# Kernel optimization log

Measured on AMD Instinct MI355X. Metric: run time of the kernel, lower is better.

## Reference

```python
import jax, jax.numpy as jnp
import numpy as np

T, B, I, H, O = 512, 128, 512, 512, 12

def setup_inputs() -> dict:
    key = jax.random.key(0)
    ks = jax.random.split(key, 17)
    def w(k, shape):
        # xavier-normal-ish init
        std = float(np.sqrt(2.0 / (shape[0] + shape[-1])))
        return jax.random.normal(k, shape, dtype=jnp.float32) * std
    return {
        "x": jax.random.normal(ks[0], (T, B, I), dtype=jnp.float32),
        "w0": w(ks[1], (O, H)), "wz": w(ks[2], (O, H)), "wr": w(ks[3], (O, H)),
        "ws": w(ks[4], (I, H)),
        "wa": w(ks[5], (H, H)), "ua": w(ks[6], (I, H)), "va": w(ks[7], (H, 1)),
        "u0": w(ks[8], (H, H)), "uz": w(ks[9], (H, H)), "ur": w(ks[10], (H, H)),
        "c0": w(ks[11], (I, H)), "cz": w(ks[12], (I, H)), "cr": w(ks[13], (I, H)),
        "fc_w": w(ks[14], (H, O)),
        "fc_b": jnp.zeros((O,), dtype=jnp.float32),
        "max_labels": 16,
    }

def reference(x, w0, wz, wr, ws, wa, ua, va, u0, uz, ur, c0, cz, cr, fc_w, fc_b, max_labels):
    # x: [T, B, I] encoder states; decode max_labels steps of a Bahdanau-attention GRU.
    s0 = jnp.tanh(x[0] @ ws)              # [B, H]
    out0 = s0 @ fc_w + fc_b               # [B, O]
    U = jnp.einsum('tbi,ih->tbh', x, ua)  # precomputed encoder projection
    va_v = va[:, 0]                       # [H]

    def step(carry, _):
        s, out = carry                                          # [B,H], [B,O]
        e = jnp.einsum('tbh,h->tb', jnp.tanh(s @ wa + U), va_v)  # [T,B] additive scores
        a = jax.nn.softmax(e, axis=0)                           # attention over T
        c = jnp.einsum('tb,tbi->bi', a, x)                      # [B,I] context
        r = jax.nn.sigmoid(out @ wr + s @ ur + c @ cr)
        z = jax.nn.sigmoid(out @ wz + s @ uz + c @ cz)
        sh = jnp.tanh(out @ w0 + (r * s) @ u0 + c @ c0)
        s_new = (1.0 - z) * s + z * sh
        out_new = s_new @ fc_w + fc_b
        return (s_new, out_new), out_new

    _, outs = jax.lax.scan(step, (s0, out0), None, length=max_labels - 1)
    all_outs = jnp.concatenate([out0[None], outs], axis=0)  # [L, B, O]
    return jnp.transpose(all_outs, (1, 0, 2))               # [B, L, O]
```

## Files before the change

### kernel.cpp

```cpp
#include <hip/hip_runtime.h>

#define NSTEP 16

typedef __attribute__((ext_vector_type(8))) short s16x8;
typedef __attribute__((ext_vector_type(4))) float f32x4;
typedef __attribute__((ext_vector_type(2))) float f32x2;

__device__ __forceinline__ float bf2f(unsigned short u){
  union { unsigned int i; float f; } v; v.i = ((unsigned int)u) << 16; return v.f;
}
__device__ __forceinline__ unsigned short f2bf(float f){
  union { float f; unsigned int i; } v; v.f = f;
  unsigned int r = v.i + 0x7fffu + ((v.i >> 16) & 1u);
  return (unsigned short)(r >> 16);
}
__device__ __forceinline__ unsigned char f2fp8(float f){
  return (unsigned char)(__builtin_amdgcn_cvt_pk_fp8_f32(f, f, 0, false) & 0xff);
}
__device__ __forceinline__ float fast_rcp(float x){ return __builtin_amdgcn_rcpf(x); }
__device__ __forceinline__ float fast_tanh(float x){
  float e = __expf(2.0f * x);
  return 1.0f - 2.0f * fast_rcp(e + 1.0f);
}
__device__ __forceinline__ float fast_sigmoid(float x){
  return fast_rcp(1.0f + __expf(-x));
}
__device__ __forceinline__ void gload16(const void* g, void* l){
  __builtin_amdgcn_global_load_lds((const __attribute__((address_space(1))) void*)g,
                                   (__attribute__((address_space(3))) void*)l, 16, 0, 0);
}
__device__ __forceinline__ float wave_sum(float v){
#pragma unroll
  for (int off = 32; off; off >>= 1) v += __shfl_xor(v, off, 64);
  return v;
}
__device__ __forceinline__ void fp8x8_dec(uint2 w, float* u){
  f32x2 d0 = __builtin_amdgcn_cvt_pk_f32_fp8(w.x, false);
  f32x2 d1 = __builtin_amdgcn_cvt_pk_f32_fp8(w.x, true);
  f32x2 d2 = __builtin_amdgcn_cvt_pk_f32_fp8(w.y, false);
  f32x2 d3 = __builtin_amdgcn_cvt_pk_f32_fp8(w.y, true);
  u[0] = d0[0]; u[1] = d0[1]; u[2] = d1[0]; u[3] = d1[1];
  u[4] = d2[0]; u[5] = d2[1]; u[6] = d3[0]; u[7] = d3[1];
}

struct GemmLDS { unsigned short A[64 * 64]; unsigned short B[128 * 64]; };

__global__ __launch_bounds__(512) void ugemm_k(
    const unsigned short* __restrict__ A, const unsigned short* __restrict__ Bt,
    unsigned char* __restrict__ o8){
  __shared__ GemmLDS lds;
  const int tid = threadIdx.x;
  const int lane = tid & 63, wid = tid >> 6;
  const int wr = wid >> 2, wc = wid & 3;
  const int mt = blockIdx.y, nt = blockIdx.x;
  f32x4 acc[2][2];
#pragma unroll
  for (int m = 0; m < 2; ++m)
#pragma unroll
    for (int n = 0; n < 2; ++n) acc[m][n] = (f32x4)0.0f;

  for (int kt = 0; kt < 512; kt += 64){
    __syncthreads();
    {
      int row = tid >> 3, kc = (tid & 7) ^ (row & 7);
      gload16(A + (size_t)(mt * 64 + row) * 512 + kt + kc * 8, &lds.A[tid * 8]);
#pragma unroll
      for (int p = 0; p < 2; ++p){
        int s = p * 512 + tid;
        int br = s >> 3, bkc = (s & 7) ^ (br & 7);
        gload16(Bt + (size_t)(nt * 128 + br) * 512 + kt + bkc * 8, &lds.B[s * 8]);
      }
    }
    __syncthreads();
#pragma unroll
    for (int ks = 0; ks < 2; ++ks){
      int kc_l = (lane >> 4) + ks * 4;
      s16x8 av[2], bv[2];
#pragma unroll
      for (int m = 0; m < 2; ++m){
        int r = wr * 32 + m * 16 + (lane & 15);
        av[m] = *(const s16x8*)&lds.A[r * 64 + ((kc_l ^ (r & 7)) << 3)];
      }
#pragma unroll
      for (int n = 0; n < 2; ++n){
        int c = wc * 32 + n * 16 + (lane & 15);
        bv[n] = *(const s16x8*)&lds.B[c * 64 + ((kc_l ^ (c & 7)) << 3)];
      }
#pragma unroll
      for (int m = 0; m < 2; ++m)
#pragma unroll
        for (int n = 0; n < 2; ++n)
          acc[m][n] = __builtin_amdgcn_mfma_f32_16x16x32_bf16(av[m], bv[n], acc[m][n], 0, 0, 0);
    }
  }
#pragma unroll
  for (int m = 0; m < 2; ++m)
#pragma unroll
    for (int n = 0; n < 2; ++n){
      int r_base = mt * 64 + wr * 32 + m * 16 + ((lane >> 4) << 2);
      int col = nt * 128 + wc * 32 + n * 16 + (lane & 15);
#pragma unroll
      for (int q = 0; q < 4; ++q)
        o8[(size_t)(r_base + q) * 512 + col] = f2fp8(acc[m][n][q]);
    }
}

struct FLDS { unsigned short A[64 * 256]; unsigned short B[64 * 256]; };

template<int EPI>
__device__ __forceinline__ void fgemm_body(int mt, int nt,
    const unsigned short* __restrict__ A, const unsigned short* __restrict__ Bt,
    unsigned short* __restrict__ ob0, float* __restrict__ o0,
    const float* __restrict__ e0, const float* __restrict__ e1,
    const float* __restrict__ e2, FLDS& lds){
  const int tid = threadIdx.x;
  const int lane = tid & 63, wid = tid >> 6;
  const int wr = wid >> 1, wc = wid & 1;
  f32x4 acc[2];
  acc[0] = (f32x4)0.0f; acc[1] = (f32x4)0.0f;

  for (int kt = 0; kt < 512; kt += 256){
    if (kt) __syncthreads();
#pragma unroll
    for (int i = 0; i < 4; ++i){
      int s = i * 512 + tid;
      int row = s >> 5, c = s & 31;
      int sc = (c & 24) | ((c & 7) ^ (row & 7));
      gload16(A + (size_t)(mt * 64 + row) * 512 + kt + sc * 8, &lds.A[s * 8]);
      gload16(Bt + (size_t)(nt * 64 + row) * 512 + kt + sc * 8, &lds.B[s * 8]);
    }
    __syncthreads();
#pragma unroll
    for (int kk = 0; kk < 8; ++kk){
      int kch = kk * 4 + (lane >> 4);
      int ar = wr * 16 + (lane & 15);
      int asw = (kch & 24) | ((kch & 7) ^ (ar & 7));
      s16x8 av = *(const s16x8*)&lds.A[ar * 256 + asw * 8];
#pragma unroll
      for (int n = 0; n < 2; ++n){
        int br = wc * 32 + n * 16 + (lane & 15);
        int bsw = (kch & 24) | ((kch & 7) ^ (br & 7));
        s16x8 bv = *(const s16x8*)&lds.B[br * 256 + bsw * 8];
        acc[n] = __builtin_amdgcn_mfma_f32_16x16x32_bf16(av, bv, acc[n], 0, 0, 0);
      }
    }
  }

#pragma unroll
  for (int n = 0; n < 2; ++n){
    int r_base = mt * 64 + wr * 16 + ((lane >> 4) << 2);
    int col = nt * 64 + wc * 32 + n * 16 + (lane & 15);
#pragma unroll
    for (int q = 0; q < 4; ++q){
      float v = acc[n][q];
      size_t r_ = (size_t)(r_base + q);
      if constexpr (EPI == 1){
        float t = fast_tanh(v);
        o0[r_ * 512 + col] = t;
        ob0[r_ * 512 + col] = f2bf(t);
      } else if constexpr (EPI == 2){
        o0[r_ * 2048 + col] = v + e0[col];
      } else if constexpr (EPI == 4){
        float v2 = v + e0[r_ * 512 + col];
        float sh = fast_tanh(v2);
        float z  = e1[r_ * 512 + col];
        float so = e2[r_ * 512 + col];
        float sn = (1.0f - z) * so + z * sh;
        o0[r_ * 512 + col] = sn;
        ob0[r_ * 512 + col] = f2bf(sn);
      }
    }
  }
}

template<int EPI>
__global__ __launch_bounds__(512) void fgemm_k(
    const unsigned short* __restrict__ A, const unsigned short* __restrict__ Bt,
    unsigned short* __restrict__ ob0, float* __restrict__ o0,
    const float* __restrict__ e0, const float* __restrict__ e1,
    const float* __restrict__ e2){
  __shared__ FLDS lds;
  fgemm_body<EPI>(blockIdx.y, blockIdx.x, A, Bt, ob0, o0, e0, e1, e2, lds);
}

__global__ __launch_bounds__(512) void ec_k(const unsigned char* __restrict__ U8,
    const unsigned char* __restrict__ x8, const float* __restrict__ pre1,
    const float* __restrict__ va, float* __restrict__ cpart, float* __restrict__ psum){
  __shared__ float cred[8][512];
  __shared__ float pred[8];
  int chunk = blockIdx.x, b = blockIdx.y;
  int tid = threadIdx.x, lane = tid & 63, wid = tid >> 6;
  const float* pp = pre1 + (size_t)b * 2048 + lane * 8;
  float4 p0 = *(const float4*)pp, p1 = *(const float4*)(pp + 4);
  const float* vp = va + lane * 8;
  float4 v0 = *(const float4*)vp, v1 = *(const float4*)(vp + 4);
  float sv[8] = {p0.x, p0.y, p0.z, p0.w, p1.x, p1.y, p1.z, p1.w};
  float vv[8] = {v0.x, v0.y, v0.z, v0.w, v1.x, v1.y, v1.z, v1.w};
  float acc[8] = {0, 0, 0, 0, 0, 0, 0, 0};
  float psum_l = 0.f;
  int t0 = chunk * 256 + wid * 32;
  for (int i = 0; i < 32; ++i){
    int t = t0 + i;
    uint2 w = *(const uint2*)(U8 + ((size_t)t * 128 + b) * 512 + lane * 8);
    float u[8];
    fp8x8_dec(w, u);
    float e = 0.f;
#pragma unroll
    for (int k = 0; k < 8; ++k)
      e += fast_tanh(u[k] + sv[k]) * vv[k];
    e = wave_sum(e);
    float p = __expf(e);
    psum_l += p;
    uint2 wx = *(const uint2*)(x8 + ((size_t)t * 128 + b) * 512 + lane * 8);
    float ux[8];
    fp8x8_dec(wx, ux);
#pragma unroll
    for (int k = 0; k < 8; ++k) acc[k] += p * ux[k];
  }
#pragma unroll
  for (int k = 0; k < 8; ++k) cred[wid][lane * 8 + k] = acc[k];
  if (lane == 0) pred[wid] = psum_l;
  __syncthreads();
  float cs = 0.f;
#pragma unroll
  for (int w = 0; w < 8; ++w) cs += cred[w][tid];
  cpart[((size_t)chunk * 128 + b) * 512 + tid] = cs;
  if (tid == 0){
    float s = 0.f;
#pragma unroll
    for (int w = 0; w < 8; ++w) s += pred[w];
    psum[chunk * 128 + b] = s;
  }
}

__global__ __launch_bounds__(512) void gates_k(
    const float* __restrict__ cpart, const float* __restrict__ psum,
    const unsigned short* __restrict__ P2w, const float* __restrict__ pre1,
    const float* __restrict__ s_prev,
    unsigned short* __restrict__ rsb, float* __restrict__ zbuf, float* __restrict__ cu0){
  __shared__ FLDS lds;
  __shared__ float rden_s[64];
  const int tid = threadIdx.x;
  const int lane = tid & 63, wid = tid >> 6;
  const int wr = wid >> 1, wc = wid & 1;
  const int nt = blockIdx.x, mt = blockIdx.y;
  if (tid < 64){
    float d = psum[mt * 64 + tid] + psum[128 + mt * 64 + tid];
    rden_s[tid] = fast_rcp(d);
  }
  f32x4 acc[2];
  acc[0] = (f32x4)0.0f; acc[1] = (f32x4)0.0f;

  for (int kt = 0; kt < 512; kt += 256){
    __syncthreads();
#pragma unroll
    for (int i = 0; i < 4; ++i){
      int s = i * 512 + tid;
      int row = s >> 5, c = s & 31;
      int sc = (c & 24) | ((c & 7) ^ (row & 7));
      int b = mt * 64 + row;
      const float* cp0 = cpart + (size_t)b * 512 + kt + sc * 8;
      const float* cp1 = cp0 + (size_t)128 * 512;
      float rd = rden_s[row];
      float4 a0 = *(const float4*)cp0, a1 = *(const float4*)(cp0 + 4);
      float4 b0 = *(const float4*)cp1, b1 = *(const float4*)(cp1 + 4);
      s16x8 t8;
      t8[0] = (short)f2bf((a0.x + b0.x) * rd); t8[1] = (short)f2bf((a0.y + b0.y) * rd);
      t8[2] = (short)f2bf((a0.z + b0.z) * rd); t8[3] = (short)f2bf((a0.w + b0.w) * rd);
      t8[4] = (short)f2bf((a1.x + b1.x) * rd); t8[5] = (short)f2bf((a1.y + b1.y) * rd);
      t8[6] = (short)f2bf((a1.z + b1.z) * rd); t8[7] = (short)f2bf((a1.w + b1.w) * rd);
      *(s16x8*)&lds.A[s * 8] = t8;
      gload16(P2w + (size_t)(nt * 64 + row) * 512 + kt + sc * 8, &lds.B[s * 8]);
    }
    __syncthreads();
#pragma unroll
    for (int kk = 0; kk < 8; ++kk){
      int kch = kk * 4 + (lane >> 4);
      int ar = wr * 16 + (lane & 15);
      int asw = (kch & 24) | ((kch & 7) ^ (ar & 7));
      s16x8 av = *(const s16x8*)&lds.A[ar * 256 + asw * 8];
#pragma unroll
      for (int n = 0; n < 2; ++n){
        int br = wc * 32 + n * 16 + (lane & 15);
        int bsw = (kch & 24) | ((kch & 7) ^ (br & 7));
        s16x8 bv = *(const s16x8*)&lds.B[br * 256 + bsw * 8];
        acc[n] = __builtin_amdgcn_mfma_f32_16x16x32_bf16(av, bv, acc[n], 0, 0, 0);
      }
    }
  }

#pragma unroll
  for (int n = 0; n < 2; ++n){
    int r_base = mt * 64 + wr * 16 + ((lane >> 4) << 2);
    int col = nt * 64 + wc * 32 + n * 16 + (lane & 15);
#pragma unroll
    for (int q = 0; q < 4; ++q){
      float v = acc[n][q];
      size_t r_ = (size_t)(r_base + q);
      float v2 = v + pre1[r_ * 2048 + 512 + col];
      if (col < 512){
        float rg = fast_sigmoid(v2);
        rsb[r_ * 512 + col] = f2bf(rg * s_prev[r_ * 512 + col]);
      } else if (col < 1024){
        zbuf[r_ * 512 + (col - 512)] = fast_sigmoid(v2);
      } else {
        cu0[r_ * 512 + (col - 1024)] = v2;
      }
    }
  }
}

__global__ __launch_bounds__(512) void dout_k(const float* __restrict__ s_hist,
    const float* __restrict__ fcwT, const float* __restrict__ fcb,
    float* __restrict__ dout){
  int lane = threadIdx.x & 63, wid = threadIdx.x >> 6;
  int w = blockIdx.x * 8 + wid;
  int step = w >> 7, b = w & 127;
  const float* sp = s_hist + (size_t)w * 512 + lane * 8;
  float4 sa = *(const float4*)sp, sb = *(const float4*)(sp + 4);
#pragma unroll
  for (int o = 0; o < 12; ++o){
    const float* fp = fcwT + (size_t)o * 512 + lane * 8;
    float4 fa = *(const float4*)fp, fb = *(const float4*)(fp + 4);
    float sum = sa.x * fa.x + sa.y * fa.y + sa.z * fa.z + sa.w * fa.w +
                sb.x * fb.x + sb.y * fb.y + sb.z * fb.z + sb.w * fb.w;
    sum = wave_sum(sum);
    if (lane == 0)
      dout[(size_t)b * (NSTEP * 12) + step * 12 + o] = sum + fcb[o];
  }
}

__global__ __launch_bounds__(256) void castx_k(const float* __restrict__ x,
    unsigned short* __restrict__ xb, unsigned char* __restrict__ x8){
  size_t idx = (size_t)blockIdx.x * 256 + threadIdx.x;
  const float* p = x + idx * 8;
  float4 a = *(const float4*)p, b = *(const float4*)(p + 4);
  s16x8 t8;
  t8[0] = (short)f2bf(a.x); t8[1] = (short)f2bf(a.y);
  t8[2] = (short)f2bf(a.z); t8[3] = (short)f2bf(a.w);
  t8[4] = (short)f2bf(b.x); t8[5] = (short)f2bf(b.y);
  t8[6] = (short)f2bf(b.z); t8[7] = (short)f2bf(b.w);
  *(s16x8*)(xb + idx * 8) = t8;
  unsigned int lo, hi;
  lo = __builtin_amdgcn_cvt_pk_fp8_f32(a.x, a.y, 0, false);
  lo = __builtin_amdgcn_cvt_pk_fp8_f32(a.z, a.w, lo, true);
  hi = __builtin_amdgcn_cvt_pk_fp8_f32(b.x, b.y, 0, false);
  hi = __builtin_amdgcn_cvt_pk_fp8_f32(b.z, b.w, hi, true);
  uint2 w; w.x = lo; w.y = hi;
  *(uint2*)(x8 + idx * 8) = w;
}

__global__ __launch_bounds__(512) void trans_k(
    const float* __restrict__ ua, const float* __restrict__ wsm,
    const float* __restrict__ u0, const float* __restrict__ wa,
    const float* __restrict__ urm, const float* __restrict__ uz,
    const float* __restrict__ cr, const float* __restrict__ cz,
    const float* __restrict__ c0, const float* __restrict__ wrm,
    const float* __restrict__ wzm, const float* __restrict__ w0m,
    const float* __restrict__ fcw, const float* __restrict__ fcb,
    unsigned short* __restrict__ Pua, unsigned short* __restrict__ Pws,
    unsigned short* __restrict__ P3w, unsigned short* __restrict__ P1w,
    unsigned short* __restrict__ P2w, float* __restrict__ fcwT,
    float* __restrict__ bias_full){
  __shared__ unsigned short tr[64][72];
  int bid = blockIdx.x, tid = threadIdx.x;
  if (bid < 640){
    int mi = bid >> 6, tile = bid & 63;
    int trr = tile >> 3, tcc = tile & 7;
    const float* src = nullptr; const float* W = nullptr; unsigned short* dst;
    switch (mi){
      case 0: src = ua;  dst = Pua;               break;
      case 1: src = wsm; dst = Pws;               break;
      case 2: src = u0;  dst = P3w;               break;
      case 3: src = wa;  dst = P1w;               break;
      case 4: src = urm; dst = P1w + 512 * 512;  W = wrm; break;
      case 5: src = uz;  dst = P1w + 1024 * 512; W = wzm; break;
      case 6: src = nullptr; dst = P1w + 1536 * 512; W = w0m; break;
      case 7: src = cr;  dst = P2w;               break;
      case 8: src = cz;  dst = P2w + 512 * 512;   break;
      default:src = c0;  dst = P2w + 1024 * 512;  break;
    }
    int r = tid >> 3, c8 = (tid & 7) * 8;
    int h = trr * 64 + r;
    float vals[8];
    if (src){
      const float* sp = src + (size_t)h * 512 + tcc * 64 + c8;
      float4 a = *(const float4*)sp, b = *(const float4*)(sp + 4);
      vals[0] = a.x; vals[1] = a.y; vals[2] = a.z; vals[3] = a.w;
      vals[4] = b.x; vals[5] = b.y; vals[6] = b.z; vals[7] = b.w;
    } else {
#pragma unroll
      for (int k = 0; k < 8; ++k) vals[k] = 0.f;
    }
    if (W){
      float fr[12];
#pragma unroll
      for (int o = 0; o < 12; ++o) fr[o] = fcw[h * 12 + o];
#pragma unroll
      for (int jj = 0; jj < 8; ++jj){
        int j = tcc * 64 + c8 + jj;
        float cj = 0.f;
#pragma unroll
        for (int o = 0; o < 12; ++o) cj += fr[o] * W[o * 512 + j];
        vals[jj] += cj;
      }
    }
    unsigned short* lp = &tr[r][c8];
#pragma unroll
    for (int k = 0; k < 8; ++k) lp[k] = f2bf(vals[k]);
    __syncthreads();
    s16x8 o8v;
#pragma unroll
    for (int k = 0; k < 8; ++k) o8v[k] = (short)tr[c8 + k][r];
    *(s16x8*)(dst + (size_t)(tcc * 64 + r) * 512 + trr * 64 + c8) = o8v;
  } else if (bid < 652){
    int gidx = (bid - 640) * 512 + tid;
    int h = gidx / 12, o = gidx - h * 12;
    fcwT[(size_t)o * 512 + h] = fcw[h * 12 + o];
  } else {
#pragma unroll
    for (int p = 0; p < 4; ++p){
      int col = p * 512 + tid;
      float v = 0.f;
      if (p > 0){
        const float* W = (p == 1) ? wrm : (p == 2) ? wzm : w0m;
#pragma unroll
        for (int o = 0; o < 12; ++o) v += fcb[o] * W[o * 512 + tid];
      }
      bias_full[col] = v;
    }
  }
}

extern "C" void kernel_launch(void* const* d_in, const int* in_sizes, int n_in,
                              void* d_out, int out_size, void* d_ws, size_t ws_size,
                              hipStream_t stream){
  const float* x   = (const float*)d_in[0];
  const float* w0  = (const float*)d_in[1];
  const float* wz  = (const float*)d_in[2];
  const float* wrm = (const float*)d_in[3];
  const float* wsm = (const float*)d_in[4];
  const float* wa  = (const float*)d_in[5];
  const float* ua  = (const float*)d_in[6];
  const float* va  = (const float*)d_in[7];
  const float* u0  = (const float*)d_in[8];
  const float* uz  = (const float*)d_in[9];
  const float* urm = (const float*)d_in[10];
  const float* c0  = (const float*)d_in[11];
  const float* cz  = (const float*)d_in[12];
  const float* cr  = (const float*)d_in[13];
  const float* fcw = (const float*)d_in[14];
  const float* fcb = (const float*)d_in[15];
  float* dout = (float*)d_out;

  char* base = (char*)d_ws;
  size_t off = 0;
  auto alloc = [&](size_t bytes) -> char* {
    char* p = base + off; off += (bytes + 255) & ~(size_t)255; return p;
  };
  unsigned short* xb   = (unsigned short*)alloc((size_t)512 * 128 * 512 * 2);
  unsigned char*  x8   = (unsigned char*) alloc((size_t)512 * 128 * 512);
  unsigned char*  U8   = (unsigned char*) alloc((size_t)512 * 128 * 512);
  unsigned short* Pua  = (unsigned short*)alloc(512 * 512 * 2);
  unsigned short* Pws  = (unsigned short*)alloc(512 * 512 * 2);
  unsigned short* P3w  = (unsigned short*)alloc(512 * 512 * 2);
  unsigned short* P1w  = (unsigned short*)alloc((size_t)2048 * 512 * 2);
  unsigned short* P2w  = (unsigned short*)alloc((size_t)1536 * 512 * 2);
  float* fcwT          = (float*)alloc(12 * 512 * 4);
  float* bias_full     = (float*)alloc(2048 * 4);
  float* pre1          = (float*)alloc((size_t)128 * 2048 * 4);
  float* cpart         = (float*)alloc((size_t)2 * 128 * 512 * 4);
  float* psum          = (float*)alloc(2 * 128 * 4);
  unsigned short* rsb  = (unsigned short*)alloc((size_t)128 * 512 * 2);
  float* zbuf          = (float*)alloc((size_t)128 * 512 * 4);
  float* cu0           = (float*)alloc((size_t)128 * 512 * 4);
  float* s_hist        = (float*)alloc((size_t)NSTEP * 128 * 512 * 4);
  unsigned short* s_bf = (unsigned short*)alloc((size_t)128 * 512 * 2);
  (void)ws_size; (void)in_sizes; (void)n_in; (void)out_size;

  castx_k<<<16384, 256, 0, stream>>>(x, xb, x8);
  trans_k<<<653, 512, 0, stream>>>(ua, wsm, u0, wa, urm, uz, cr, cz, c0,
                                   wrm, wz, w0, fcw, fcb,
                                   Pua, Pws, P3w, P1w, P2w, fcwT, bias_full);
  ugemm_k<<<dim3(4, 1024), 512, 0, stream>>>(xb, Pua, U8);
  fgemm_k<1><<<dim3(8, 2), 512, 0, stream>>>(xb, Pws, s_bf, s_hist,
                                             nullptr, nullptr, nullptr);

  for (int step = 1; step < NSTEP; ++step){
    const float* s_prev = s_hist + (size_t)(step - 1) * 128 * 512;
    float* s_cur = s_hist + (size_t)step * 128 * 512;
    fgemm_k<2><<<dim3(32, 2), 512, 0, stream>>>(s_bf, P1w, nullptr, pre1,
                                                bias_full, nullptr, nullptr);
    ec_k<<<dim3(2, 128), 512, 0, stream>>>(U8, x8, pre1, va, cpart, psum);
    gates_k<<<dim3(24, 2), 512, 0, stream>>>(cpart, psum, P2w, pre1, s_prev,
                                             rsb, zbuf, cu0);
    fgemm_k<4><<<dim3(8, 2), 512, 0, stream>>>(rsb, P3w, s_bf, s_cur,
                                               cu0, zbuf, s_prev);
  }
  dout_k<<<256, 512, 0, stream>>>(s_hist, fcwT, fcb, dout);
}
```

Before: 800.6 us.

## Fuse per-step projection GEMM and attention kernel into one launch

Merges the per-step pre-projection GEMM and the attention/context kernel into a single launch with 304 blocks. The first 48 blocks compute the gate projections (ur/uz/u0 paths). The remaining blocks each recompute s@wa for their batch row with scalar FMAs from a bf16 copy of wa, then do the attention pass. This removes one kernel launch and a dependency per decode step, but every attention block redundantly computes a 512x512 matvec (twice per batch row) on CUDA cores. The bias and weight packing are reorganised to match.

```diff
diff --git a/kernel.cpp b/kernel.cpp
--- a/kernel.cpp
+++ b/kernel.cpp
@@ -159,7 +159,7 @@
         o0[r_ * 512 + col] = t;
         ob0[r_ * 512 + col] = f2bf(t);
       } else if constexpr (EPI == 2){
-        o0[r_ * 2048 + col] = v + e0[col];
+        o0[r_ * 1536 + col] = v + e0[col];
       } else if constexpr (EPI == 4){
         float v2 = v + e0[r_ * 512 + col];
         float sh = fast_tanh(v2);
@@ -183,19 +183,66 @@
   fgemm_body<EPI>(blockIdx.y, blockIdx.x, A, Bt, ob0, o0, e0, e1, e2, lds);
 }
 
-__global__ __launch_bounds__(512) void ec_k(const unsigned char* __restrict__ U8,
-    const unsigned char* __restrict__ x8, const float* __restrict__ pre1,
-    const float* __restrict__ va, float* __restrict__ cpart, float* __restrict__ psum){
-  __shared__ float cred[8][512];
-  __shared__ float pred[8];
-  int chunk = blockIdx.x, b = blockIdx.y;
-  int tid = threadIdx.x, lane = tid & 63, wid = tid >> 6;
-  const float* pp = pre1 + (size_t)b * 2048 + lane * 8;
-  float4 p0 = *(const float4*)pp, p1 = *(const float4*)(pp + 4);
-  const float* vp = va + lane * 8;
-  float4 v0 = *(const float4*)vp, v1 = *(const float4*)(vp + 4);
-  float sv[8] = {p0.x, p0.y, p0.z, p0.w, p1.x, p1.y, p1.z, p1.w};
-  float vv[8] = {v0.x, v0.y, v0.z, v0.w, v1.x, v1.y, v1.z, v1.w};
+union MidLDS {
+  FLDS g;
+  struct {
+    float part[8][512];
+    float s_s[512];
+    float pre_wa[512];
+    float pred[8];
+  } e;
+};
+
+__global__ __launch_bounds__(512) void mid_k(
+    const unsigned char* __restrict__ U8, const unsigned char* __restrict__ x8,
+    const unsigned short* __restrict__ s_bf, const unsigned short* __restrict__ PwaNT,
+    const unsigned short* __restrict__ P23w, const float* __restrict__ bias23,
+    const float* __restrict__ va,
+    float* __restrict__ pre23, float* __restrict__ cpart, float* __restrict__ psum){
+  __shared__ MidLDS lds;
+  const int bid = blockIdx.x, tid = threadIdx.x;
+  const int lane = tid & 63, wid = tid >> 6;
+
+  if (bid < 48){
+    fgemm_body<2>(bid & 1, bid >> 1, s_bf, P23w, nullptr, pre23,
+                  bias23, nullptr, nullptr, lds.g);
+    return;
+  }
+  const int eb = bid - 48;
+  const int chunk = eb >> 7, b = eb & 127;
+
+  lds.e.s_s[tid] = bf2f(s_bf[(size_t)b * 512 + tid]);
+  __syncthreads();
+  {
+    float pacc[8] = {0, 0, 0, 0, 0, 0, 0, 0};
+    for (int kk = 0; kk < 64; ++kk){
+      int k = wid * 64 + kk;
+      float sv = lds.e.s_s[k];
+      s16x8 wv = *(const s16x8*)&PwaNT[(size_t)k * 512 + lane * 8];
+#pragma unroll
+      for (int j = 0; j < 8; ++j) pacc[j] += sv * bf2f((unsigned short)wv[j]);
+    }
+#pragma unroll
+    for (int j = 0; j < 8; ++j) lds.e.part[wid][lane * 8 + j] = pacc[j];
+  }
+  __syncthreads();
+  {
+    float s = 0.f;
+#pragma unroll
+    for (int g = 0; g < 8; ++g) s += lds.e.part[g][tid];
+    lds.e.pre_wa[tid] = s;
+  }
+  __syncthreads();
+
+  float sv[8], vv[8];
+  {
+    const float* vp = va + lane * 8;
+    float4 v0 = *(const float4*)vp, v1 = *(const float4*)(vp + 4);
+    vv[0] = v0.x; vv[1] = v0.y; vv[2] = v0.z; vv[3] = v0.w;
+    vv[4] = v1.x; vv[5] = v1.y; vv[6] = v1.z; vv[7] = v1.w;
+#pragma unroll
+    for (int j = 0; j < 8; ++j) sv[j] = lds.e.pre_wa[lane * 8 + j];
+  }
   float acc[8] = {0, 0, 0, 0, 0, 0, 0, 0};
   float psum_l = 0.f;
   int t0 = chunk * 256 + wid * 32;
@@ -217,25 +264,26 @@
 #pragma unroll
     for (int k = 0; k < 8; ++k) acc[k] += p * ux[k];
   }
-#pragma unroll
-  for (int k = 0; k < 8; ++k) cred[wid][lane * 8 + k] = acc[k];
-  if (lane == 0) pred[wid] = psum_l;
+  __syncthreads();
+#pragma unroll
+  for (int k = 0; k < 8; ++k) lds.e.part[wid][lane * 8 + k] = acc[k];
+  if (lane == 0) lds.e.pred[wid] = psum_l;
   __syncthreads();
   float cs = 0.f;
 #pragma unroll
-  for (int w = 0; w < 8; ++w) cs += cred[w][tid];
+  for (int g = 0; g < 8; ++g) cs += lds.e.part[g][tid];
   cpart[((size_t)chunk * 128 + b) * 512 + tid] = cs;
   if (tid == 0){
     float s = 0.f;
 #pragma unroll
-    for (int w = 0; w < 8; ++w) s += pred[w];
+    for (int g = 0; g < 8; ++g) s += lds.e.pred[g];
     psum[chunk * 128 + b] = s;
   }
 }
 
 __global__ __launch_bounds__(512) void gates_k(
     const float* __restrict__ cpart, const float* __restrict__ psum,
-    const unsigned short* __restrict__ P2w, const float* __restrict__ pre1,
+    const unsigned short* __restrict__ P2w, const float* __restrict__ pre23,
     const float* __restrict__ s_prev,
     unsigned short* __restrict__ rsb, float* __restrict__ zbuf, float* __restrict__ cu0){
   __shared__ FLDS lds;
@@ -297,7 +345,7 @@
     for (int q = 0; q < 4; ++q){
       float v = acc[n][q];
       size_t r_ = (size_t)(r_base + q);
-      float v2 = v + pre1[r_ * 2048 + 512 + col];
+      float v2 = v + pre23[r_ * 1536 + col];
       if (col < 512){
         float rg = fast_sigmoid(v2);
         rsb[r_ * 512 + col] = f2bf(rg * s_prev[r_ * 512 + col]);
@@ -359,12 +407,12 @@
     const float* __restrict__ wzm, const float* __restrict__ w0m,
     const float* __restrict__ fcw, const float* __restrict__ fcb,
     unsigned short* __restrict__ Pua, unsigned short* __restrict__ Pws,
-    unsigned short* __restrict__ P3w, unsigned short* __restrict__ P1w,
-    unsigned short* __restrict__ P2w, float* __restrict__ fcwT,
-    float* __restrict__ bias_full){
+    unsigned short* __restrict__ P3w, unsigned short* __restrict__ P23w,
+    unsigned short* __restrict__ P2w, unsigned short* __restrict__ PwaNT,
+    float* __restrict__ fcwT, float* __restrict__ bias23){
   __shared__ unsigned short tr[64][72];
   int bid = blockIdx.x, tid = threadIdx.x;
-  if (bid < 640){
+  if (bid < 576){
     int mi = bid >> 6, tile = bid & 63;
     int trr = tile >> 3, tcc = tile & 7;
     const float* src = nullptr; const float* W = nullptr; unsigned short* dst;
@@ -372,12 +420,11 @@
       case 0: src = ua;  dst = Pua;               break;
       case 1: src = wsm; dst = Pws;               break;
       case 2: src = u0;  dst = P3w;               break;
-      case 3: src = wa;  dst = P1w;               break;
-      case 4: src = urm; dst = P1w + 512 * 512;  W = wrm; break;
-      case 5: src = uz;  dst = P1w + 1024 * 512; W = wzm; break;
-      case 6: src = nullptr; dst = P1w + 1536 * 512; W = w0m; break;
-      case 7: src = cr;  dst = P2w;               break;
-      case 8: src = cz;  dst = P2w + 512 * 512;   break;
+      case 3: src = urm; dst = P23w;              W = wrm; break;
+      case 4: src = uz;  dst = P23w + 512 * 512;  W = wzm; break;
+      case 5: src = nullptr; dst = P23w + 1024 * 512; W = w0m; break;
+      case 6: src = cr;  dst = P2w;               break;
+      case 7: src = cz;  dst = P2w + 512 * 512;   break;
       default:src = c0;  dst = P2w + 1024 * 512;  break;
     }
     int r = tid >> 3, c8 = (tid & 7) * 8;
@@ -413,22 +460,27 @@
 #pragma unroll
     for (int k = 0; k < 8; ++k) o8v[k] = (short)tr[c8 + k][r];
     *(s16x8*)(dst + (size_t)(tcc * 64 + r) * 512 + trr * 64 + c8) = o8v;
+  } else if (bid < 640){
+    size_t idx = (size_t)(bid - 576) * 512 + tid;
+    const float* p = wa + idx * 8;
+    float4 a = *(const float4*)p, b = *(const float4*)(p + 4);
+    s16x8 t8;
+    t8[0] = (short)f2bf(a.x); t8[1] = (short)f2bf(a.y);
+    t8[2] = (short)f2bf(a.z); t8[3] = (short)f2bf(a.w);
+    t8[4] = (short)f2bf(b.x); t8[5] = (short)f2bf(b.y);
+    t8[6] = (short)f2bf(b.z); t8[7] = (short)f2bf(b.w);
+    *(s16x8*)(PwaNT + idx * 8) = t8;
   } else if (bid < 652){
     int gidx = (bid - 640) * 512 + tid;
     int h = gidx / 12, o = gidx - h * 12;
     fcwT[(size_t)o * 512 + h] = fcw[h * 12 + o];
   } else {
-#pragma unroll
-    for (int p = 0; p < 4; ++p){
-      int col = p * 512 + tid;
-      float v = 0.f;
-      if (p > 0){
-        const float* W = (p == 1) ? wrm : (p == 2) ? wzm : w0m;
-#pragma unroll
-        for (int o = 0; o < 12; ++o) v += fcb[o] * W[o * 512 + tid];
-      }
-      bias_full[col] = v;
-    }
+    int p = bid - 652;
+    const float* W = (p == 0) ? wrm : (p == 1) ? wzm : w0m;
+    float v = 0.f;
+#pragma unroll
+    for (int o = 0; o < 12; ++o) v += fcb[o] * W[o * 512 + tid];
+    bias23[p * 512 + tid] = v;
   }
 }
 
@@ -464,11 +516,12 @@
   unsigned short* Pua  = (unsigned short*)alloc(512 * 512 * 2);
   unsigned short* Pws  = (unsigned short*)alloc(512 * 512 * 2);
   unsigned short* P3w  = (unsigned short*)alloc(512 * 512 * 2);
-  unsigned short* P1w  = (unsigned short*)alloc((size_t)2048 * 512 * 2);
+  unsigned short* P23w = (unsigned short*)alloc((size_t)1536 * 512 * 2);
   unsigned short* P2w  = (unsigned short*)alloc((size_t)1536 * 512 * 2);
+  unsigned short* PwaNT= (unsigned short*)alloc(512 * 512 * 2);
   float* fcwT          = (float*)alloc(12 * 512 * 4);
-  float* bias_full     = (float*)alloc(2048 * 4);
-  float* pre1          = (float*)alloc((size_t)128 * 2048 * 4);
+  float* bias23        = (float*)alloc(1536 * 4);
+  float* pre23         = (float*)alloc((size_t)128 * 1536 * 4);
   float* cpart         = (float*)alloc((size_t)2 * 128 * 512 * 4);
   float* psum          = (float*)alloc(2 * 128 * 4);
   unsigned short* rsb  = (unsigned short*)alloc((size_t)128 * 512 * 2);
@@ -479,9 +532,9 @@
   (void)ws_size; (void)in_sizes; (void)n_in; (void)out_size;
 
   castx_k<<<16384, 256, 0, stream>>>(x, xb, x8);
-  trans_k<<<653, 512, 0, stream>>>(ua, wsm, u0, wa, urm, uz, cr, cz, c0,
+  trans_k<<<655, 512, 0, stream>>>(ua, wsm, u0, wa, urm, uz, cr, cz, c0,
                                    wrm, wz, w0, fcw, fcb,
-                                   Pua, Pws, P3w, P1w, P2w, fcwT, bias_full);
+                                   Pua, Pws, P3w, P23w, P2w, PwaNT, fcwT, bias23);
   ugemm_k<<<dim3(4, 1024), 512, 0, stream>>>(xb, Pua, U8);
   fgemm_k<1><<<dim3(8, 2), 512, 0, stream>>>(xb, Pws, s_bf, s_hist,
                                              nullptr, nullptr, nullptr);
@@ -489,10 +542,9 @@
   for (int step = 1; step < NSTEP; ++step){
     const float* s_prev = s_hist + (size_t)(step - 1) * 128 * 512;
     float* s_cur = s_hist + (size_t)step * 128 * 512;
-    fgemm_k<2><<<dim3(32, 2), 512, 0, stream>>>(s_bf, P1w, nullptr, pre1,
-                                                bias_full, nullptr, nullptr);
-    ec_k<<<dim3(2, 128), 512, 0, stream>>>(U8, x8, pre1, va, cpart, psum);
-    gates_k<<<dim3(24, 2), 512, 0, stream>>>(cpart, psum, P2w, pre1, s_prev,
+    mid_k<<<304, 512, 0, stream>>>(U8, x8, s_bf, PwaNT, P23w, bias23, va,
+                                   pre23, cpart, psum);
+    gates_k<<<dim3(24, 2), 512, 0, stream>>>(cpart, psum, P2w, pre23, s_prev,
                                              rsb, zbuf, cu0);
     fgemm_k<4><<<dim3(8, 2), 512, 0, stream>>>(rsb, P3w, s_bf, s_cur,
                                                cu0, zbuf, s_prev);
```

Result: slower. 884.0 us (+10.4%).

## Fuse state-update GEMM with next-step projection and split attention over more chunks

Applied to the files above, without the earlier changes.

Adds a new spre_k kernel. Each block redundantly computes every state tile for its batch tile with the EPI=4 epilogue, then runs two tiles of the next step's pre-projection GEMM. This removes one launch and one dependency per step, at the cost of duplicated GEMM work and benign duplicate writes of the same values. Separately, the attention kernel now splits T into 8 chunks of 64 with 256-thread blocks, giving more blocks to spread across CUs. gates_k now reduces 8 partial context sums instead of 2, which adds some extra memory traffic.

```diff
diff --git a/kernel.cpp b/kernel.cpp
--- a/kernel.cpp
+++ b/kernel.cpp
@@ -183,11 +183,30 @@
   fgemm_body<EPI>(blockIdx.y, blockIdx.x, A, Bt, ob0, o0, e0, e1, e2, lds);
 }
 
-__global__ __launch_bounds__(512) void ec_k(const unsigned char* __restrict__ U8,
+__global__ __launch_bounds__(512) void spre_k(
+    const unsigned short* __restrict__ rsb, const unsigned short* __restrict__ P3w,
+    const unsigned short* __restrict__ P1w, const float* __restrict__ bias_full,
+    const float* __restrict__ cu0, const float* __restrict__ zbuf,
+    const float* __restrict__ s_prev, float* __restrict__ s_cur,
+    unsigned short* __restrict__ s_bf, float* __restrict__ pre1){
+  __shared__ FLDS lds;
+  const int mt = blockIdx.x >> 4, g = blockIdx.x & 15;
+  for (int nt2 = 0; nt2 < 8; ++nt2){
+    fgemm_body<4>(mt, nt2, rsb, P3w, s_bf, s_cur, cu0, zbuf, s_prev, lds);
+    __syncthreads();
+  }
+  for (int j = 0; j < 2; ++j){
+    fgemm_body<2>(mt, g * 2 + j, s_bf, P1w, nullptr, pre1,
+                  bias_full, nullptr, nullptr, lds);
+    __syncthreads();
+  }
+}
+
+__global__ __launch_bounds__(256) void ec_k(const unsigned char* __restrict__ U8,
     const unsigned char* __restrict__ x8, const float* __restrict__ pre1,
     const float* __restrict__ va, float* __restrict__ cpart, float* __restrict__ psum){
-  __shared__ float cred[8][512];
-  __shared__ float pred[8];
+  __shared__ float cred[4][512];
+  __shared__ float pred[4];
   int chunk = blockIdx.x, b = blockIdx.y;
   int tid = threadIdx.x, lane = tid & 63, wid = tid >> 6;
   const float* pp = pre1 + (size_t)b * 2048 + lane * 8;
@@ -198,8 +217,8 @@
   float vv[8] = {v0.x, v0.y, v0.z, v0.w, v1.x, v1.y, v1.z, v1.w};
   float acc[8] = {0, 0, 0, 0, 0, 0, 0, 0};
   float psum_l = 0.f;
-  int t0 = chunk * 256 + wid * 32;
-  for (int i = 0; i < 32; ++i){
+  int t0 = chunk * 64 + wid * 16;
+  for (int i = 0; i < 16; ++i){
     int t = t0 + i;
     uint2 w = *(const uint2*)(U8 + ((size_t)t * 128 + b) * 512 + lane * 8);
     float u[8];
@@ -221,16 +240,13 @@
   for (int k = 0; k < 8; ++k) cred[wid][lane * 8 + k] = acc[k];
   if (lane == 0) pred[wid] = psum_l;
   __syncthreads();
-  float cs = 0.f;
-#pragma unroll
-  for (int w = 0; w < 8; ++w) cs += cred[w][tid];
-  cpart[((size_t)chunk * 128 + b) * 512 + tid] = cs;
-  if (tid == 0){
-    float s = 0.f;
-#pragma unroll
-    for (int w = 0; w < 8; ++w) s += pred[w];
-    psum[chunk * 128 + b] = s;
-  }
+#pragma unroll
+  for (int j = 0; j < 2; ++j){
+    int col = j * 256 + tid;
+    cpart[((size_t)chunk * 128 + b) * 512 + col] =
+        cred[0][col] + cred[1][col] + cred[2][col] + cred[3][col];
+  }
+  if (tid == 0) psum[chunk * 128 + b] = pred[0] + pred[1] + pred[2] + pred[3];
 }
 
 __global__ __launch_bounds__(512) void gates_k(
@@ -245,7 +261,9 @@
   const int wr = wid >> 1, wc = wid & 1;
   const int nt = blockIdx.x, mt = blockIdx.y;
   if (tid < 64){
-    float d = psum[mt * 64 + tid] + psum[128 + mt * 64 + tid];
+    float d = 0.f;
+#pragma unroll
+    for (int ch = 0; ch < 8; ++ch) d += psum[ch * 128 + mt * 64 + tid];
     rden_s[tid] = fast_rcp(d);
   }
   f32x4 acc[2];
@@ -259,16 +277,18 @@
       int row = s >> 5, c = s & 31;
       int sc = (c & 24) | ((c & 7) ^ (row & 7));
       int b = mt * 64 + row;
-      const float* cp0 = cpart + (size_t)b * 512 + kt + sc * 8;
-      const float* cp1 = cp0 + (size_t)128 * 512;
       float rd = rden_s[row];
-      float4 a0 = *(const float4*)cp0, a1 = *(const float4*)(cp0 + 4);
-      float4 b0 = *(const float4*)cp1, b1 = *(const float4*)(cp1 + 4);
+      float vsum[8] = {0, 0, 0, 0, 0, 0, 0, 0};
+#pragma unroll
+      for (int ch = 0; ch < 8; ++ch){
+        const float* cp = cpart + ((size_t)ch * 128 + b) * 512 + kt + sc * 8;
+        float4 a0 = *(const float4*)cp, a1 = *(const float4*)(cp + 4);
+        vsum[0] += a0.x; vsum[1] += a0.y; vsum[2] += a0.z; vsum[3] += a0.w;
+        vsum[4] += a1.x; vsum[5] += a1.y; vsum[6] += a1.z; vsum[7] += a1.w;
+      }
       s16x8 t8;
-      t8[0] = (short)f2bf((a0.x + b0.x) * rd); t8[1] = (short)f2bf((a0.y + b0.y) * rd);
-      t8[2] = (short)f2bf((a0.z + b0.z) * rd); t8[3] = (short)f2bf((a0.w + b0.w) * rd);
-      t8[4] = (short)f2bf((a1.x + b1.x) * rd); t8[5] = (short)f2bf((a1.y + b1.y) * rd);
-      t8[6] = (short)f2bf((a1.z + b1.z) * rd); t8[7] = (short)f2bf((a1.w + b1.w) * rd);
+#pragma unroll
+      for (int k = 0; k < 8; ++k) t8[k] = (short)f2bf(vsum[k] * rd);
       *(s16x8*)&lds.A[s * 8] = t8;
       gload16(P2w + (size_t)(nt * 64 + row) * 512 + kt + sc * 8, &lds.B[s * 8]);
     }
@@ -469,8 +489,8 @@
   float* fcwT          = (float*)alloc(12 * 512 * 4);
   float* bias_full     = (float*)alloc(2048 * 4);
   float* pre1          = (float*)alloc((size_t)128 * 2048 * 4);
-  float* cpart         = (float*)alloc((size_t)2 * 128 * 512 * 4);
-  float* psum          = (float*)alloc(2 * 128 * 4);
+  float* cpart         = (float*)alloc((size_t)8 * 128 * 512 * 4);
+  float* psum          = (float*)alloc(8 * 128 * 4);
   unsigned short* rsb  = (unsigned short*)alloc((size_t)128 * 512 * 2);
   float* zbuf          = (float*)alloc((size_t)128 * 512 * 4);
   float* cu0           = (float*)alloc((size_t)128 * 512 * 4);
@@ -485,17 +505,17 @@
   ugemm_k<<<dim3(4, 1024), 512, 0, stream>>>(xb, Pua, U8);
   fgemm_k<1><<<dim3(8, 2), 512, 0, stream>>>(xb, Pws, s_bf, s_hist,
                                              nullptr, nullptr, nullptr);
+  fgemm_k<2><<<dim3(32, 2), 512, 0, stream>>>(s_bf, P1w, nullptr, pre1,
+                                              bias_full, nullptr, nullptr);
 
   for (int step = 1; step < NSTEP; ++step){
     const float* s_prev = s_hist + (size_t)(step - 1) * 128 * 512;
     float* s_cur = s_hist + (size_t)step * 128 * 512;
-    fgemm_k<2><<<dim3(32, 2), 512, 0, stream>>>(s_bf, P1w, nullptr, pre1,
-                                                bias_full, nullptr, nullptr);
-    ec_k<<<dim3(2, 128), 512, 0, stream>>>(U8, x8, pre1, va, cpart, psum);
+    ec_k<<<dim3(8, 128), 256, 0, stream>>>(U8, x8, pre1, va, cpart, psum);
     gates_k<<<dim3(24, 2), 512, 0, stream>>>(cpart, psum, P2w, pre1, s_prev,
                                              rsb, zbuf, cu0);
-    fgemm_k<4><<<dim3(8, 2), 512, 0, stream>>>(rsb, P3w, s_bf, s_cur,
-                                               cu0, zbuf, s_prev);
+    spre_k<<<32, 512, 0, stream>>>(rsb, P3w, P1w, bias_full, cu0, zbuf,
+                                   s_prev, s_cur, s_bf, pre1);
   }
   dout_k<<<256, 512, 0, stream>>>(s_hist, fcwT, fcb, dout);
 }
```

New measurement: 1.616 ms. 2.02x slower.
